# Kernel tuning notes

Hardware: AMD Instinct MI355X
Metric: run time of the kernel (lower is better)

The kernel has to match this reference:

```python
import jax, jax.numpy as jnp
import numpy as np

NHEAD = 16
NEG1 = -9e15   # first masked_fill value (-9000000000000000.0)
NEG2 = -9e16   # second masked_fill value


def setup_inputs() -> dict:
    key = jax.random.key(0)
    ks = jax.random.split(key, 8)
    slen, bsz, emb = 512, 16, 1024
    x = jax.random.normal(ks[0], (slen, bsz, emb), dtype=jnp.float32)
    mask = jax.random.randint(ks[1], (bsz, slen, slen), 0, 2, dtype=jnp.int32)
    weight_mask = jax.random.randint(ks[2], (bsz, slen, slen), 0, 2, dtype=jnp.int32)
    s = 1.0 / np.sqrt(emb)
    Wq = jax.random.normal(ks[3], (emb, emb), dtype=jnp.float32) * s
    Wk = jax.random.normal(ks[4], (emb, emb), dtype=jnp.float32) * s
    Wv = jax.random.normal(ks[5], (emb, emb), dtype=jnp.float32) * s
    Ws = jax.random.normal(ks[6], (emb, emb), dtype=jnp.float32) * s
    Wb = jax.random.normal(ks[7], (1, 3 * emb), dtype=jnp.float32) * s
    return {"x": x, "mask": mask, "weight_mask": weight_mask,
            "Wq": Wq, "Wk": Wk, "Wv": Wv, "Ws": Ws, "Wb": Wb}


def reference(x, mask, weight_mask, Wq, Wk, Wv, Ws, Wb):
    slen, bsz, emb = x.shape
    hd = emb // NHEAD
    scaling = float(hd) ** -0.5

    def split_heads(t):  # (slen, bsz, emb) -> (bsz, nhead, slen, hd)
        return t.reshape(slen, bsz, NHEAD, hd).transpose(1, 2, 0, 3)

    q = split_heads(x @ Wq.T)
    k = split_heads(x @ Wk.T)
    v = split_heads(x @ Wv.T)

    attn = jnp.einsum('bhqd,bhkd->bhqk', q, k) * scaling

    m = mask.astype(attn.dtype)[:, None, :, :]          # (bsz,1,slen,slen)
    attn = jnp.where(m == 0, NEG1, attn)
    attn = jax.nn.softmax(attn, axis=-1) * m

    wm = weight_mask.astype(attn.dtype)[:, None, :, :]
    attn = jnp.where(wm == 0, NEG2, attn)
    attn = jax.nn.softmax(attn, axis=-1) * wm
    # degree normalization: row-normalize
    attn = attn * (1.0 / (attn.sum(-1) + 1e-10))[..., None]

    # dropout inactive (eval mode)
    out = jnp.einsum('bhqk,bhkd->bhqd', attn, v)         # (bsz,nhead,slen,hd)
    out = out.transpose(2, 0, 1, 3).reshape(slen, bsz, emb)

    r = x @ Ws.T
    gate = jax.nn.sigmoid(jnp.concatenate([out, r, out - r], axis=-1) @ Wb.T)
    return gate * r + (1.0 - gate) * out
```

## Files before the change

kernel.cpp:

```cpp
#include <hip/hip_runtime.h>
#include <hip/hip_bf16.h>
#include <stdint.h>

typedef __attribute__((ext_vector_type(8))) short short8;
typedef __attribute__((ext_vector_type(4))) float f32x4;
typedef __attribute__((ext_vector_type(4))) unsigned short ushort4v;

#define MFMA_BF16(a,b,c) __builtin_amdgcn_mfma_f32_16x16x32_bf16((a),(b),(c),0,0,0)

static __device__ __forceinline__ unsigned short f2bf(float f){
  union { float fv; unsigned int u; } c; c.fv = f;
  unsigned int u = c.u;
  return (unsigned short)((u + 0x7fffu + ((u >> 16) & 1u)) >> 16);
}

static __device__ __forceinline__ unsigned int cvtpk(float a, float b){
  unsigned int r;
  asm("v_cvt_pk_bf16_f32 %0, %1, %2" : "=v"(r) : "v"(a), "v"(b));
  return r;
}

static __device__ __forceinline__ void gload_lds16(const void* g, void* l){
  __builtin_amdgcn_global_load_lds(
      (const __attribute__((address_space(1))) void*)g,
      (__attribute__((address_space(3))) void*)l, 16, 0, 0);
}

static __device__ __forceinline__ float wred_sum(float v){
  #pragma unroll
  for (int m = 32; m; m >>= 1) v += __shfl_xor(v, m, 64);
  return v;
}

static __device__ __forceinline__ void unpack8(uint4 u, float* f){
  f[0] = __uint_as_float(u.x << 16); f[1] = __uint_as_float(u.x & 0xFFFF0000u);
  f[2] = __uint_as_float(u.y << 16); f[3] = __uint_as_float(u.y & 0xFFFF0000u);
  f[4] = __uint_as_float(u.z << 16); f[5] = __uint_as_float(u.z & 0xFFFF0000u);
  f[6] = __uint_as_float(u.w << 16); f[7] = __uint_as_float(u.w & 0xFFFF0000u);
}

__global__ __launch_bounds__(256) void cvt_x_kernel(const float* __restrict__ x,
                                                    unsigned short* __restrict__ o){
  int i = blockIdx.x * 256 + threadIdx.x;
  float4 f = ((const float4*)x)[i];
  ushort4v r;
  r[0] = f2bf(f.x); r[1] = f2bf(f.y); r[2] = f2bf(f.z); r[3] = f2bf(f.w);
  ((ushort4v*)o)[i] = r;
}

__global__ __launch_bounds__(256) void cvt_w_kernel(const float* __restrict__ Wq,
                                                    const float* __restrict__ Wk,
                                                    const float* __restrict__ Wv,
                                                    const float* __restrict__ Ws,
                                                    unsigned short* __restrict__ B){
  int i = blockIdx.x * 256 + threadIdx.x;
  int which = i >> 18;
  const float* src = (which == 0) ? Wq : (which == 1) ? Wk : (which == 2) ? Wv : Ws;
  float4 f = ((const float4*)src)[i & 262143];
  ushort4v r;
  r[0] = f2bf(f.x); r[1] = f2bf(f.y); r[2] = f2bf(f.z); r[3] = f2bf(f.w);
  ((ushort4v*)B)[i] = r;
}

__global__ void wb_prep_kernel(const float* __restrict__ Wb,
                               float* __restrict__ wba, float* __restrict__ wbb){
  int e = blockIdx.x * 256 + threadIdx.x;
  if (e < 1024){
    wba[e] = Wb[e]        + Wb[2048 + e];
    wbb[e] = Wb[1024 + e] - Wb[2048 + e];
  }
}

__global__ __launch_bounds__(256) void mask_prep_kernel(
    const int* __restrict__ m, const int* __restrict__ wm,
    unsigned long long* __restrict__ mb, unsigned long long* __restrict__ wb)
{
  const size_t i = (size_t)blockIdx.x * 256 + threadIdx.x;
  const int a = m[i];
  const int c = wm[i];
  unsigned long long ba = __ballot(a != 0);
  unsigned long long bc = __ballot(c != 0);
  if ((threadIdx.x & 63) == 0){
    mb[i >> 6] = ba;
    wb[i >> 6] = bc;
  }
}

__global__ __launch_bounds__(512, 1) void gemm_proj_kernel(
    const unsigned short* __restrict__ X, const unsigned short* __restrict__ B,
    unsigned short* __restrict__ qb, unsigned short* __restrict__ kb,
    unsigned short* __restrict__ vT, unsigned short* __restrict__ rbb)
{
  __shared__ __align__(16) unsigned short smem[73728];
  const int tid = threadIdx.x;
  const int w = tid >> 6, l = tid & 63;
  const int lr = l & 15, lq = l >> 4;
  const int wm = w >> 1, wn = w & 1;
  const int bid = ((blockIdx.x & 7) << 7) | (blockIdx.x >> 3);
  const int mt = bid >> 5, nt = bid & 31;
  const int m0 = mt * 256, n0 = nt * 128;
  const int lrow8 = l >> 3, lc = l & 7;

  f32x4 acc[4][4] = {};

  #define STAGE(T) { \
    const int bufo_ = ((T) % 3) * 24576; \
    const int kk_ = (T) * 64; \
    _Pragma("unroll") \
    for (int j = 0; j < 4; j++){ \
      const int seg = w + j * 8; \
      const int r = seg * 8 + lrow8; \
      gload_lds16(X + (size_t)(m0 + r) * 1024 + kk_ + ((lc ^ (r & 7)) * 8), \
                  smem + bufo_ + seg * 512); \
    } \
    _Pragma("unroll") \
    for (int j = 0; j < 2; j++){ \
      const int seg = w + j * 8; \
      const int r = seg * 8 + lrow8; \
      gload_lds16(B + (size_t)(n0 + r) * 1024 + kk_ + ((lc ^ (r & 7)) * 8), \
                  smem + bufo_ + 16384 + seg * 512); \
    } }

  #define COMPUTE(T) { \
    const int bo_ = ((T) % 3) * 24576; \
    _Pragma("unroll") \
    for (int subk = 0; subk < 2; subk++){ \
      short8 av[4], bv[4]; \
      const int pc = (((subk * 4 + lq) ^ (lr & 7)) * 8); \
      _Pragma("unroll") \
      for (int mf = 0; mf < 4; mf++) \
        av[mf] = *(const short8*)(smem + bo_ + (wm * 64 + mf * 16 + lr) * 64 + pc); \
      _Pragma("unroll") \
      for (int nf = 0; nf < 4; nf++) \
        bv[nf] = *(const short8*)(smem + bo_ + 16384 + (wn * 64 + nf * 16 + lr) * 64 + pc); \
      __builtin_amdgcn_s_setprio(1); \
      _Pragma("unroll") \
      for (int mf = 0; mf < 4; mf++) \
        _Pragma("unroll") \
        for (int nf = 0; nf < 4; nf++) \
          acc[mf][nf] = MFMA_BF16(av[mf], bv[nf], acc[mf][nf]); \
      __builtin_amdgcn_s_setprio(0); \
    } }

  STAGE(0)
  STAGE(1)

  for (int t = 0; t < 15; t++){
    asm volatile("s_waitcnt vmcnt(6)" ::: "memory");
    __builtin_amdgcn_s_barrier();
    if (t < 14) STAGE(t + 2)
    COMPUTE(t)
  }
  asm volatile("s_waitcnt vmcnt(0)" ::: "memory");
  __builtin_amdgcn_s_barrier();
  COMPUTE(15)

  const int which = nt >> 3;
  const int o0 = (nt & 7) * 128;
  if (which == 2){
    __syncthreads();
    #pragma unroll
    for (int mf = 0; mf < 4; mf++)
      #pragma unroll
      for (int nf = 0; nf < 4; nf++){
        const int c = wn * 64 + nf * 16 + lr;
        const int r0v = wm * 64 + mf * 16 + lq * 4;
        uint2 pk;
        pk.x = cvtpk(acc[mf][nf][0], acc[mf][nf][1]);
        pk.y = cvtpk(acc[mf][nf][2], acc[mf][nf][3]);
        *(uint2*)(smem + c * 264 + r0v) = pk;
      }
    __syncthreads();
    #pragma unroll
    for (int p = 0; p < 8; p++){
      const int cid = p * 512 + tid;
      const int c = cid >> 5, bb = (cid >> 1) & 15, sh = cid & 1;
      short8 st;
      #pragma unroll
      for (int j = 0; j < 8; j++) st[j] = (short)smem[c * 264 + (sh * 8 + j) * 16 + bb];
      const int o = o0 + c;
      const int bh = bb * 16 + (o >> 6), d = o & 63;
      *(short8*)(vT + ((size_t)bh * 64 + d) * 512 + mt * 16 + sh * 8) = st;
    }
  } else {
    #pragma unroll
    for (int h2 = 0; h2 < 2; h2++){
      __syncthreads();
      if ((wm >> 1) == h2){
        #pragma unroll
        for (int mf = 0; mf < 4; mf++)
          #pragma unroll
          for (int nf = 0; nf < 4; nf++)
            #pragma unroll
            for (int rg = 0; rg < 4; rg++)
              smem[((wm & 1) * 64 + mf * 16 + lq * 4 + rg) * 136 + wn * 64 + nf * 16 + lr]
                  = f2bf(acc[mf][nf][rg]);
      }
      __syncthreads();
      if (which == 3){
        #pragma unroll
        for (int p = 0; p < 4; p++){
          const int cid = p * 512 + tid;
          const int lrow = cid >> 4, cg = cid & 15;
          short8 vv = *(const short8*)(smem + lrow * 136 + cg * 8);
          *(short8*)(rbb + (size_t)(m0 + h2 * 128 + lrow) * 1024 + o0 + cg * 8) = vv;
        }
      } else {
        unsigned short* dst = (which == 0) ? qb : kb;
        #pragma unroll
        for (int p = 0; p < 4; p++){
          const int cid = p * 512 + tid;
          const int lrow = cid >> 4, cg = cid & 15;
          short8 vv = *(const short8*)(smem + lrow * 136 + cg * 8);
          const int rowi = m0 + h2 * 128 + lrow;
          const int s = rowi >> 4, bb = rowi & 15;
          const int o = o0 + cg * 8;
          const int bh = bb * 16 + (o >> 6), d = o & 63;
          *(short8*)(dst + ((size_t)bh * 512 + s) * 64 + d) = vv;
        }
      }
    }
  }
  #undef STAGE
  #undef COMPUTE
}

__global__ __launch_bounds__(256, 4) void attn_kernel(
    const unsigned short* __restrict__ qg, const unsigned short* __restrict__ kg,
    const unsigned short* __restrict__ vt,
    const unsigned char* __restrict__ mbits, const unsigned char* __restrict__ wbits,
    unsigned short* __restrict__ outp)
{
  __shared__ __align__(16) unsigned short sE[32 * 520];
  __shared__ float sfin[32];
  const int bid = ((blockIdx.x & 7) << 9) | (blockIdx.x >> 3);
  const int qt = bid & 15, h = (bid >> 4) & 15, b = bid >> 8;
  const int tid = threadIdx.x, w = tid >> 6, l = tid & 63;
  const int lr = l & 15, lq = l >> 4;
  const int bh = b * 16 + h;
  const unsigned short* qp = qg + ((size_t)bh * 512 + qt * 32) * 64;
  const unsigned short* kp = kg + (size_t)bh * 512 * 64;
  const unsigned short* vp = vt + (size_t)bh * 64 * 512;

  const unsigned char* mrb = mbits + ((size_t)(b * 512 + qt * 32)) * 64;
  const unsigned char* wrb = wbits + ((size_t)(b * 512 + qt * 32)) * 64;
  unsigned int mby[2][4], wby[2][4];
  #pragma unroll
  for (int g = 0; g < 2; g++)
    #pragma unroll
    for (int rr = 0; rr < 4; rr++){
      mby[g][rr] = mrb[(g * 16 + w * 4 + rr) * 64 + l];
      wby[g][rr] = wrb[(g * 16 + w * 4 + rr) * 64 + l];
    }

  short8 qa[2][2];
  #pragma unroll
  for (int t = 0; t < 2; t++){
    qa[t][0] = *(const short8*)(qp + (t * 16 + lr) * 64 + lq * 8);
    qa[t][1] = *(const short8*)(qp + (t * 16 + lr) * 64 + 32 + lq * 8);
  }
  const float CEXP = 0.18033688011112042f;
  #pragma unroll
  for (int kf = 0; kf < 8; kf++){
    const unsigned short* kr = kp + (size_t)(w * 128 + kf * 16 + lr) * 64;
    short8 k0 = *(const short8*)(kr + lq * 8);
    short8 k1 = *(const short8*)(kr + 32 + lq * 8);
    f32x4 a0 = {}, a1 = {};
    a0 = MFMA_BF16(qa[0][0], k0, a0);
    a1 = MFMA_BF16(qa[1][0], k0, a1);
    a0 = MFMA_BF16(qa[0][1], k1, a0);
    a1 = MFMA_BF16(qa[1][1], k1, a1);
    const int col = w * 128 + kf * 16 + lr;
    #pragma unroll
    for (int t = 0; t < 2; t++){
      f32x4 a = t ? a1 : a0;
      float e0 = __builtin_amdgcn_exp2f(a[0] * CEXP);
      float e1 = __builtin_amdgcn_exp2f(a[1] * CEXP);
      float e2 = __builtin_amdgcn_exp2f(a[2] * CEXP);
      float e3 = __builtin_amdgcn_exp2f(a[3] * CEXP);
      unsigned int p01 = cvtpk(e0, e1), p23 = cvtpk(e2, e3);
      const int row = t * 16 + lq * 4;
      sE[(row    ) * 520 + col] = (unsigned short)(p01 & 0xFFFFu);
      sE[(row + 1) * 520 + col] = (unsigned short)(p01 >> 16);
      sE[(row + 2) * 520 + col] = (unsigned short)(p23 & 0xFFFFu);
      sE[(row + 3) * 520 + col] = (unsigned short)(p23 >> 16);
    }
  }
  __syncthreads();

  #pragma unroll
  for (int g = 0; g < 2; g++){
    const int row0 = g * 16 + w * 4;
    uint4 ev[4];
    #pragma unroll
    for (int rr = 0; rr < 4; rr++)
      ev[rr] = *(const uint4*)(sE + (row0 + rr) * 520 + l * 8);

    float em[4][8]; float z1[4];
    #pragma unroll
    for (int rr = 0; rr < 4; rr++){
      float e1[8];
      unpack8(ev[rr], e1);
      const unsigned int mb = mby[g][rr];
      float z = 0.f;
      #pragma unroll
      for (int j = 0; j < 8; j++){
        em[rr][j] = ((mb >> j) & 1u) ? e1[j] : 0.f;
        z += em[rr][j];
      }
      z1[rr] = z;
    }
    #pragma unroll
    for (int m = 32; m; m >>= 1){
      #pragma unroll
      for (int rr = 0; rr < 4; rr++) z1[rr] += __shfl_xor(z1[rr], m, 64);
    }
    float e2[4][8]; float z2[4];
    #pragma unroll
    for (int rr = 0; rr < 4; rr++){
      const float i1L = 1.4426950408889634f / z1[rr];
      const unsigned int wv = wby[g][rr];
      float z = 0.f;
      #pragma unroll
      for (int j = 0; j < 8; j++){
        float t = __builtin_amdgcn_exp2f(em[rr][j] * i1L);
        e2[rr][j] = ((wv >> j) & 1u) ? t : 0.f;
        z += e2[rr][j];
      }
      z2[rr] = z;
    }
    #pragma unroll
    for (int m = 32; m; m >>= 1){
      #pragma unroll
      for (int rr = 0; rr < 4; rr++) z2[rr] += __shfl_xor(z2[rr], m, 64);
    }
    #pragma unroll
    for (int rr = 0; rr < 4; rr++){
      uint4 o;
      o.x = cvtpk(e2[rr][0], e2[rr][1]); o.y = cvtpk(e2[rr][2], e2[rr][3]);
      o.z = cvtpk(e2[rr][4], e2[rr][5]); o.w = cvtpk(e2[rr][6], e2[rr][7]);
      *(uint4*)(sE + (row0 + rr) * 520 + l * 8) = o;
      if (l == 0) sfin[row0 + rr] = 1.f / (z2[rr] + 1e-10f);
    }
  }
  __syncthreads();

  {
    f32x4 po0 = {}, po1 = {};
    #pragma unroll
    for (int ks = 0; ks < 16; ks++){
      short8 vf = *(const short8*)(vp + (size_t)(w * 16 + lr) * 512 + ks * 32 + lq * 8);
      short8 af0 = *(const short8*)(sE + (     lr) * 520 + ks * 32 + lq * 8);
      short8 af1 = *(const short8*)(sE + (16 + lr) * 520 + ks * 32 + lq * 8);
      po0 = MFMA_BF16(af0, vf, po0);
      po1 = MFMA_BF16(af1, vf, po1);
    }
    #pragma unroll
    for (int rg = 0; rg < 4; rg++){
      const int r0 = lq * 4 + rg;
      outp[((size_t)(qt * 32 + r0) * 16 + b) * 1024 + h * 64 + w * 16 + lr]
          = f2bf(po0[rg] * sfin[r0]);
      outp[((size_t)(qt * 32 + 16 + r0) * 16 + b) * 1024 + h * 64 + w * 16 + lr]
          = f2bf(po1[rg] * sfin[16 + r0]);
    }
  }
}

__global__ __launch_bounds__(256) void gate_kernel(
    const unsigned short* __restrict__ outp, const unsigned short* __restrict__ rbb,
    const float* __restrict__ wba, const float* __restrict__ wbb,
    float* __restrict__ y)
{
  const int t = blockIdx.x * 4 + (threadIdx.x >> 6);
  const int l = threadIdx.x & 63;
  const unsigned short* o = outp + (size_t)t * 1024;
  const unsigned short* r = rbb + (size_t)t * 1024;
  float ov[16], rv[16];
  float acc = 0.f;
  #pragma unroll
  for (int j = 0; j < 16; j++){
    const int e = j * 64 + l;
    ov[j] = __uint_as_float((unsigned int)o[e] << 16);
    rv[j] = __uint_as_float((unsigned int)r[e] << 16);
    acc += ov[j] * wba[e] + rv[j] * wbb[e];
  }
  const float dot = wred_sum(acc);
  const float g = 1.f / (1.f + __builtin_amdgcn_exp2f(-dot * 1.4426950408889634f));
  float* yo = y + (size_t)t * 1024;
  #pragma unroll
  for (int j = 0; j < 16; j++){
    const int e = j * 64 + l;
    yo[e] = g * rv[j] + (1.f - g) * ov[j];
  }
}

extern "C" void kernel_launch(void* const* d_in, const int* in_sizes, int n_in,
                              void* d_out, int out_size, void* d_ws, size_t ws_size,
                              hipStream_t stream)
{
  (void)in_sizes; (void)n_in; (void)out_size; (void)ws_size;
  const float* x   = (const float*)d_in[0];
  const int* mask  = (const int*)d_in[1];
  const int* wmask = (const int*)d_in[2];
  const float* Wq  = (const float*)d_in[3];
  const float* Wk  = (const float*)d_in[4];
  const float* Wv  = (const float*)d_in[5];
  const float* Ws  = (const float*)d_in[6];
  const float* Wb  = (const float*)d_in[7];

  char* ws = (char*)d_ws;
  unsigned short* xbf = (unsigned short*)ws; ws += 16777216;
  unsigned short* bm  = (unsigned short*)ws; ws += 8388608;
  unsigned short* qb  = (unsigned short*)ws; ws += 16777216;
  unsigned short* kb  = (unsigned short*)ws; ws += 16777216;
  unsigned short* vT  = (unsigned short*)ws; ws += 16777216;
  unsigned short* rbb = (unsigned short*)ws; ws += 16777216;
  unsigned short* op  = (unsigned short*)ws; ws += 16777216;
  float* wba = (float*)ws; ws += 4096;
  float* wbb = (float*)ws; ws += 4096;
  unsigned long long* mb64 = (unsigned long long*)xbf;
  unsigned long long* wb64 = (unsigned long long*)bm;

  cvt_x_kernel<<<8192, 256, 0, stream>>>(x, xbf);
  cvt_w_kernel<<<4096, 256, 0, stream>>>(Wq, Wk, Wv, Ws, bm);
  wb_prep_kernel<<<4, 256, 0, stream>>>(Wb, wba, wbb);
  gemm_proj_kernel<<<1024, 512, 0, stream>>>(xbf, bm, qb, kb, vT, rbb);
  mask_prep_kernel<<<16384, 256, 0, stream>>>(mask, wmask, mb64, wb64);
  attn_kernel<<<4096, 256, 0, stream>>>(qb, kb, vT,
      (const unsigned char*)mb64, (const unsigned char*)wb64, op);
  gate_kernel<<<2048, 256, 0, stream>>>(op, rbb, wba, wbb, (float*)d_out);
}
```

Baseline: 185.4 us.

## Split projection GEMM k-step into two phases interleaving staged loads with MFMA

Each k-tile of the projection GEMM is now split into two sub-k phases. Each phase reads its LDS fragments, issues half of the next-next tile's global-to-LDS loads, waits on lgkmcnt, and runs 16 MFMAs, with a barrier between the two phases. The block-to-tile mapping also changes so that each XCD handles four adjacent M tiles across all N tiles, aiming for better L2 reuse of X. The extra barrier per k-step and the forced lgkmcnt(0) waits could add stalls.

```diff
diff --git a/kernel.cpp b/kernel.cpp
--- a/kernel.cpp
+++ b/kernel.cpp
@@ -96,64 +96,66 @@
   const int w = tid >> 6, l = tid & 63;
   const int lr = l & 15, lq = l >> 4;
   const int wm = w >> 1, wn = w & 1;
-  const int bid = ((blockIdx.x & 7) << 7) | (blockIdx.x >> 3);
-  const int mt = bid >> 5, nt = bid & 31;
+  const int xcd = blockIdx.x & 7, o = blockIdx.x >> 3;
+  const int mt = xcd * 4 + (o & 3), nt = o >> 2;
   const int m0 = mt * 256, n0 = nt * 128;
   const int lrow8 = l >> 3, lc = l & 7;
 
   f32x4 acc[4][4] = {};
 
-  #define STAGE(T) { \
+  #define STAGE_H(T, H) { \
     const int bufo_ = ((T) % 3) * 24576; \
     const int kk_ = (T) * 64; \
     _Pragma("unroll") \
-    for (int j = 0; j < 4; j++){ \
+    for (int j = (H) * 2; j < (H) * 2 + 2; j++){ \
       const int seg = w + j * 8; \
       const int r = seg * 8 + lrow8; \
       gload_lds16(X + (size_t)(m0 + r) * 1024 + kk_ + ((lc ^ (r & 7)) * 8), \
                   smem + bufo_ + seg * 512); \
     } \
-    _Pragma("unroll") \
-    for (int j = 0; j < 2; j++){ \
-      const int seg = w + j * 8; \
+    { \
+      const int seg = w + (H) * 8; \
       const int r = seg * 8 + lrow8; \
       gload_lds16(B + (size_t)(n0 + r) * 1024 + kk_ + ((lc ^ (r & 7)) * 8), \
                   smem + bufo_ + 16384 + seg * 512); \
     } }
 
-  #define COMPUTE(T) { \
+  #define PHASE(T, SUBK, DOSTAGE) { \
     const int bo_ = ((T) % 3) * 24576; \
+    short8 av[4], bv[4]; \
+    const int pc = ((((SUBK) * 4 + lq) ^ (lr & 7)) * 8); \
     _Pragma("unroll") \
-    for (int subk = 0; subk < 2; subk++){ \
-      short8 av[4], bv[4]; \
-      const int pc = (((subk * 4 + lq) ^ (lr & 7)) * 8); \
-      _Pragma("unroll") \
-      for (int mf = 0; mf < 4; mf++) \
-        av[mf] = *(const short8*)(smem + bo_ + (wm * 64 + mf * 16 + lr) * 64 + pc); \
+    for (int mf = 0; mf < 4; mf++) \
+      av[mf] = *(const short8*)(smem + bo_ + (wm * 64 + mf * 16 + lr) * 64 + pc); \
+    _Pragma("unroll") \
+    for (int nf = 0; nf < 4; nf++) \
+      bv[nf] = *(const short8*)(smem + bo_ + 16384 + (wn * 64 + nf * 16 + lr) * 64 + pc); \
+    if (DOSTAGE) STAGE_H((T) + 2, SUBK) \
+    asm volatile("s_waitcnt lgkmcnt(0)" ::: "memory"); \
+    __builtin_amdgcn_sched_barrier(0); \
+    __builtin_amdgcn_s_setprio(1); \
+    _Pragma("unroll") \
+    for (int mf = 0; mf < 4; mf++) \
       _Pragma("unroll") \
       for (int nf = 0; nf < 4; nf++) \
-        bv[nf] = *(const short8*)(smem + bo_ + 16384 + (wn * 64 + nf * 16 + lr) * 64 + pc); \
-      __builtin_amdgcn_s_setprio(1); \
-      _Pragma("unroll") \
-      for (int mf = 0; mf < 4; mf++) \
-        _Pragma("unroll") \
-        for (int nf = 0; nf < 4; nf++) \
-          acc[mf][nf] = MFMA_BF16(av[mf], bv[nf], acc[mf][nf]); \
-      __builtin_amdgcn_s_setprio(0); \
-    } }
-
-  STAGE(0)
-  STAGE(1)
+        acc[mf][nf] = MFMA_BF16(av[mf], bv[nf], acc[mf][nf]); \
+    __builtin_amdgcn_s_setprio(0); }
+
+  STAGE_H(0, 0) STAGE_H(0, 1)
+  STAGE_H(1, 0) STAGE_H(1, 1)
 
   for (int t = 0; t < 15; t++){
     asm volatile("s_waitcnt vmcnt(6)" ::: "memory");
     __builtin_amdgcn_s_barrier();
-    if (t < 14) STAGE(t + 2)
-    COMPUTE(t)
+    const bool st = (t < 14);
+    PHASE(t, 0, st)
+    __builtin_amdgcn_s_barrier();
+    PHASE(t, 1, st)
   }
   asm volatile("s_waitcnt vmcnt(0)" ::: "memory");
   __builtin_amdgcn_s_barrier();
-  COMPUTE(15)
+  PHASE(15, 0, false)
+  PHASE(15, 1, false)
 
   const int which = nt >> 3;
   const int o0 = (nt & 7) * 128;
@@ -178,8 +180,8 @@
       short8 st;
       #pragma unroll
       for (int j = 0; j < 8; j++) st[j] = (short)smem[c * 264 + (sh * 8 + j) * 16 + bb];
-      const int o = o0 + c;
-      const int bh = bb * 16 + (o >> 6), d = o & 63;
+      const int oo = o0 + c;
+      const int bh = bb * 16 + (oo >> 6), d = oo & 63;
       *(short8*)(vT + ((size_t)bh * 64 + d) * 512 + mt * 16 + sh * 8) = st;
     }
   } else {
@@ -214,15 +216,15 @@
           short8 vv = *(const short8*)(smem + lrow * 136 + cg * 8);
           const int rowi = m0 + h2 * 128 + lrow;
           const int s = rowi >> 4, bb = rowi & 15;
-          const int o = o0 + cg * 8;
-          const int bh = bb * 16 + (o >> 6), d = o & 63;
+          const int oo = o0 + cg * 8;
+          const int bh = bb * 16 + (oo >> 6), d = oo & 63;
           *(short8*)(dst + ((size_t)bh * 512 + s) * 64 + d) = vv;
         }
       }
     }
   }
-  #undef STAGE
-  #undef COMPUTE
+  #undef STAGE_H
+  #undef PHASE
 }
 
 __global__ __launch_bounds__(256, 4) void attn_kernel(
@@ -336,10 +338,10 @@
     }
     #pragma unroll
     for (int rr = 0; rr < 4; rr++){
-      uint4 o;
-      o.x = cvtpk(e2[rr][0], e2[rr][1]); o.y = cvtpk(e2[rr][2], e2[rr][3]);
-      o.z = cvtpk(e2[rr][4], e2[rr][5]); o.w = cvtpk(e2[rr][6], e2[rr][7]);
-      *(uint4*)(sE + (row0 + rr) * 520 + l * 8) = o;
+      uint4 oo;
+      oo.x = cvtpk(e2[rr][0], e2[rr][1]); oo.y = cvtpk(e2[rr][2], e2[rr][3]);
+      oo.z = cvtpk(e2[rr][4], e2[rr][5]); oo.w = cvtpk(e2[rr][6], e2[rr][7]);
+      *(uint4*)(sE + (row0 + rr) * 520 + l * 8) = oo;
       if (l == 0) sfin[row0 + rr] = 1.f / (z2[rr] + 1e-10f);
     }
   }
```

New measurement: 177.8 us. 4.1% less time.
